# Performance work log

Hardware: AMD Instinct MI355X
Metric: run time of the kernel (lower is better)

Reference implementation:

```python
import jax, jax.numpy as jnp
import numpy as np

SEQ, D_IN, D_OUT = 8192, 768, 128


def setup_inputs() -> dict:
    key = jax.random.key(0)
    k1, k2, k3, k4 = jax.random.split(key, 4)
    x = jax.random.normal(k1, (SEQ, D_IN), dtype=jnp.float32)
    # torch nn.Linear weights are stored as [d_out, d_in]
    scale = 1.0 / np.sqrt(D_IN)
    w_query = jax.random.normal(k2, (D_OUT, D_IN), dtype=jnp.float32) * scale
    w_key = jax.random.normal(k3, (D_OUT, D_IN), dtype=jnp.float32) * scale
    w_value = jax.random.normal(k4, (D_OUT, D_IN), dtype=jnp.float32) * scale
    return {"x": x, "w_query": w_query, "w_key": w_key, "w_value": w_value}


def reference(x, w_query, w_key, w_value):
    # Linear with bias=False: y = x @ W.T   (W is [d_out, d_in])
    q = x @ w_query.T                      # [N, d_out]
    k = x @ w_key.T                        # [N, d_out]
    v = x @ w_value.T                      # [N, d_out]
    inv_sqrt_d = 1.0 / jnp.sqrt(jnp.float32(k.shape[-1]))
    scores = (q @ k.T) * inv_sqrt_d        # [N, N] -- fully materialized, as in source
    weights = jax.nn.softmax(scores, axis=-1)
    return weights @ v                     # [N, d_out]
```

## Files before the change

### kernel.cpp

```cpp
#include <hip/hip_runtime.h>
#include <stdint.h>

#define SEQ 8192
#define DIN 768
#define DOUT 128

typedef __attribute__((ext_vector_type(8))) short short8;
typedef __attribute__((ext_vector_type(8))) unsigned short ushort8v;
typedef __attribute__((ext_vector_type(4))) float f32x4;
typedef __attribute__((ext_vector_type(4))) unsigned int u32x4;

#define CEXPF (1.4426950408889634f * 0.08838834764831845f)

#if __has_builtin(__builtin_amdgcn_exp2f)
#define EXP2(x) __builtin_amdgcn_exp2f(x)
#else
#define EXP2(x) __builtin_exp2f(x)
#endif

__device__ __forceinline__ unsigned short f2bf(float f) {
  return (unsigned short)((__float_as_uint(f) + 0x8000u) >> 16);
}

__launch_bounds__(256, 2)
__global__ void qkv_kernel(const float* __restrict__ x,
                           const float* __restrict__ wq,
                           const float* __restrict__ wk,
                           const float* __restrict__ wvp,
                           unsigned short* __restrict__ Qb,
                           unsigned short* __restrict__ Kb,
                           unsigned short* __restrict__ Vtb) {
  __shared__ unsigned short smem[16640];
  unsigned short* xs  = smem;
  unsigned short* wsm = smem + 5120;

  const int t    = threadIdx.x;
  const int wid  = t >> 6;
  const int lane = t & 63;
  const int g    = lane >> 4;
  const int r    = lane & 15;
  const int z    = blockIdx.y;
  const int m0   = blockIdx.x * 128;
  const float* W = (z == 0) ? wq : (z == 1) ? wk : wvp;

  f32x4 acc[2][8];
#pragma unroll
  for (int i = 0; i < 2; i++)
#pragma unroll
    for (int j = 0; j < 8; j++) acc[i][j] = 0.f;

  const int srow = t >> 3;
  const int scol = (t & 7) * 4;

#pragma unroll 1
  for (int kb = 0; kb < DIN; kb += 32) {
    float4 xv[4], wv4[4];
#pragma unroll
    for (int u = 0; u < 4; u++) {
      int row = srow + u * 32;
      xv[u]  = *(const float4*)(x + (size_t)(m0 + row) * DIN + kb + scol);
      wv4[u] = *(const float4*)(W + (size_t)row * DIN + kb + scol);
    }
#pragma unroll
    for (int u = 0; u < 4; u++) {
      int row = srow + u * 32;
      ushort4 a, b;
      a.x = f2bf(xv[u].x);  a.y = f2bf(xv[u].y);
      a.z = f2bf(xv[u].z);  a.w = f2bf(xv[u].w);
      b.x = f2bf(wv4[u].x); b.y = f2bf(wv4[u].y);
      b.z = f2bf(wv4[u].z); b.w = f2bf(wv4[u].w);
      *(ushort4*)&xs[row * 40 + scol]  = a;
      *(ushort4*)&wsm[row * 40 + scol] = b;
    }
    __syncthreads();
    short8 af[2];
#pragma unroll
    for (int tm = 0; tm < 2; tm++)
      af[tm] = *(const short8*)&xs[(wid * 32 + tm * 16 + r) * 40 + g * 8];
#pragma unroll
    for (int tn = 0; tn < 8; tn++) {
      short8 bf = *(const short8*)&wsm[(tn * 16 + r) * 40 + g * 8];
      acc[0][tn] = __builtin_amdgcn_mfma_f32_16x16x32_bf16(af[0], bf, acc[0][tn], 0, 0, 0);
      acc[1][tn] = __builtin_amdgcn_mfma_f32_16x16x32_bf16(af[1], bf, acc[1][tn], 0, 0, 0);
    }
    __syncthreads();
  }

  if (z < 2) {
    unsigned short* out = (z == 0) ? Qb : Kb;
    const float sc = (z == 0) ? CEXPF : 1.0f;
#pragma unroll
    for (int tm = 0; tm < 2; tm++)
#pragma unroll
      for (int tn = 0; tn < 8; tn++)
#pragma unroll
        for (int rr = 0; rr < 4; rr++) {
          int row = m0 + wid * 32 + tm * 16 + g * 4 + rr;
          int col = tn * 16 + r;
          out[(size_t)row * DOUT + col] = f2bf(acc[tm][tn][rr] * sc);
        }
  } else {
    unsigned short* ct = smem;
#pragma unroll
    for (int tm = 0; tm < 2; tm++)
#pragma unroll
      for (int tn = 0; tn < 8; tn++)
#pragma unroll
        for (int rr = 0; rr < 4; rr++) {
          int m   = wid * 32 + tm * 16 + g * 4 + rr;
          int col = tn * 16 + r;
          ct[m * 130 + col] = f2bf(acc[tm][tn][rr]);
        }
    __syncthreads();
    int n  = t >> 1;
    int mh = (t & 1) * 64;
#pragma unroll
    for (int j = 0; j < 8; j++) {
      ushort8v vv;
#pragma unroll
      for (int i = 0; i < 8; i++) vv[i] = ct[(mh + j * 8 + i) * 130 + n];
      *(ushort8v*)(Vtb + (size_t)n * SEQ + m0 + mh + j * 8) = vv;
    }
  }
}

__launch_bounds__(256, 2)
__global__ void attn_kernel(const unsigned short* __restrict__ Qb,
                            const unsigned short* __restrict__ Kb,
                            const unsigned short* __restrict__ Vtb,
                            float* __restrict__ Opart,
                            float* __restrict__ lpart) {
  __shared__ unsigned char lds[51200];
  unsigned char* Kl = lds;
  unsigned char* Vl = lds + 16384;

  const int t    = threadIdx.x;
  const int wave = t >> 6;
  const int lane = t & 63;
  const int g    = lane >> 4;
  const int r    = lane & 15;
  unsigned short* Pl = (unsigned short*)(lds + 32768 + wave * 4608);

  const int qb = blockIdx.x;
  const int sp = blockIdx.y;
  const int q0 = qb * 128 + wave * 32;

  short8 qf[2][4];
#pragma unroll
  for (int s = 0; s < 2; s++)
#pragma unroll
    for (int c = 0; c < 4; c++)
      qf[s][c] = *(const short8*)(Qb + (size_t)(q0 + s * 16 + r) * DOUT + c * 32 + g * 8);

  short8 onesf;
#pragma unroll
  for (int j = 0; j < 8; j++) onesf[j] = (r == 0) ? (short)0x3F80 : (short)0;

  f32x4 oacc[2][8];
  f32x4 lacc[2];
#pragma unroll
  for (int s = 0; s < 2; s++) {
    lacc[s] = 0.f;
#pragma unroll
    for (int n = 0; n < 8; n++) oacc[s][n] = 0.f;
  }

#pragma unroll 1
  for (int it = 0; it < 16; it++) {
    const int kv0 = sp * 1024 + it * 64;
    {
      const u32x4* ksrc = (const u32x4*)(Kb + (size_t)kv0 * DOUT);
      u32x4 kv[4], vv[4];
#pragma unroll
      for (int j = 0; j < 4; j++) {
        int ci = t + 256 * j;
        kv[j] = ksrc[ci];
        int d = ci >> 3, cc = ci & 7;
        vv[j] = *(const u32x4*)(Vtb + (size_t)d * SEQ + kv0 + cc * 8);
      }
#pragma unroll
      for (int j = 0; j < 4; j++) {
        int ci = t + 256 * j;
        int row = ci >> 4, cc = ci & 15;
        *(u32x4*)(Kl + row * 256 + ((cc ^ (row & 15)) << 4)) = kv[j];
        int d = ci >> 3, c2 = ci & 7;
        *(u32x4*)(Vl + d * 128 + ((c2 ^ (d & 7)) << 4)) = vv[j];
      }
    }
    __syncthreads();

    f32x4 sf[2][4];
#pragma unroll
    for (int s = 0; s < 2; s++)
#pragma unroll
      for (int tt = 0; tt < 4; tt++) sf[s][tt] = 0.f;
#pragma unroll
    for (int tt = 0; tt < 4; tt++) {
      int row = tt * 16 + r;
#pragma unroll
      for (int c = 0; c < 4; c++) {
        int cc = c * 4 + g;
        short8 kf = *(const short8*)(Kl + row * 256 + ((cc ^ (row & 15)) << 4));
        sf[0][tt] = __builtin_amdgcn_mfma_f32_16x16x32_bf16(qf[0][c], kf, sf[0][tt], 0, 0, 0);
        sf[1][tt] = __builtin_amdgcn_mfma_f32_16x16x32_bf16(qf[1][c], kf, sf[1][tt], 0, 0, 0);
      }
    }

#pragma unroll
    for (int s = 0; s < 2; s++)
#pragma unroll
      for (int tt = 0; tt < 4; tt++)
#pragma unroll
        for (int rr = 0; rr < 4; rr++) {
          float p = EXP2(sf[s][tt][rr]);
          Pl[(s * 16 + g * 4 + rr) * 72 + tt * 16 + r] = f2bf(p);
        }
    short8 pf[2][2];
#pragma unroll
    for (int s = 0; s < 2; s++)
#pragma unroll
      for (int c2 = 0; c2 < 2; c2++)
        pf[s][c2] = *(const short8*)(Pl + (s * 16 + r) * 72 + c2 * 32 + g * 8);

#pragma unroll
    for (int nt = 0; nt < 8; nt++) {
      int d = nt * 16 + r;
#pragma unroll
      for (int c2 = 0; c2 < 2; c2++) {
        int cc = c2 * 4 + g;
        short8 vf = *(const short8*)(Vl + d * 128 + ((cc ^ (d & 7)) << 4));
        oacc[0][nt] = __builtin_amdgcn_mfma_f32_16x16x32_bf16(pf[0][c2], vf, oacc[0][nt], 0, 0, 0);
        oacc[1][nt] = __builtin_amdgcn_mfma_f32_16x16x32_bf16(pf[1][c2], vf, oacc[1][nt], 0, 0, 0);
      }
    }
#pragma unroll
    for (int s = 0; s < 2; s++) {
      lacc[s] = __builtin_amdgcn_mfma_f32_16x16x32_bf16(pf[s][0], onesf, lacc[s], 0, 0, 0);
      lacc[s] = __builtin_amdgcn_mfma_f32_16x16x32_bf16(pf[s][1], onesf, lacc[s], 0, 0, 0);
    }
    __syncthreads();
  }

  const size_t pbase = (size_t)sp * SEQ;
#pragma unroll
  for (int s = 0; s < 2; s++)
#pragma unroll
    for (int rr = 0; rr < 4; rr++) {
      int qrow = q0 + s * 16 + g * 4 + rr;
#pragma unroll
      for (int nt = 0; nt < 8; nt++)
        Opart[(pbase + qrow) * DOUT + nt * 16 + r] = oacc[s][nt][rr];
      if (r == 0) lpart[pbase + qrow] = lacc[s][rr];
    }
}

__global__ void combine_kernel(const float* __restrict__ Opart,
                               const float* __restrict__ lpart,
                               float* __restrict__ out) {
  int idx = blockIdx.x * 256 + threadIdx.x;
  int s   = idx >> 5;
  int d4  = (idx & 31) * 4;
  float L = 0.f;
  f32x4 acc = 0.f;
#pragma unroll
  for (int p = 0; p < 8; p++) {
    L += lpart[p * SEQ + s];
    acc += *(const f32x4*)(Opart + ((size_t)p * SEQ + s) * DOUT + d4);
  }
  f32x4 res = acc * (1.0f / L);
  *(f32x4*)(out + (size_t)s * DOUT + d4) = res;
}

extern "C" void kernel_launch(void* const* d_in, const int* in_sizes, int n_in,
                              void* d_out, int out_size, void* d_ws, size_t ws_size,
                              hipStream_t stream) {
  const float* x  = (const float*)d_in[0];
  const float* wq = (const float*)d_in[1];
  const float* wk = (const float*)d_in[2];
  const float* wv = (const float*)d_in[3];
  float* out = (float*)d_out;

  unsigned short* Qb  = (unsigned short*)d_ws;
  unsigned short* Kb  = Qb + (size_t)SEQ * DOUT;
  unsigned short* Vtb = Kb + (size_t)SEQ * DOUT;
  float* Opart = (float*)(Vtb + (size_t)SEQ * DOUT);
  float* lpart = Opart + (size_t)8 * SEQ * DOUT;
  if (ws_size < (size_t)(6291456 + 33554432 + 262144)) return;

  qkv_kernel<<<dim3(64, 3), 256, 0, stream>>>(x, wq, wk, wv, Qb, Kb, Vtb);
  attn_kernel<<<dim3(64, 8), 256, 0, stream>>>(Qb, Kb, Vtb, Opart, lpart);
  combine_kernel<<<dim3(1024), 256, 0, stream>>>(Opart, lpart, out);
}
```

Before: 149.0 us.

## Preconvert weights to bf16, retile QKV projection, use direct global-to-LDS loads in attention

Adds a small kernel that converts the three weight matrices to bf16 once per call, folding the softmax scale into Wq, and stores them in the Opart workspace before that buffer is reused. The QKV projection switches to 32-row tiles with a 256x3 grid and computes the transposed product, reading weight fragments straight from global memory. The attention kernel stages K and V with global_load_lds, swizzling on the global-address side, and swaps the QK^T operand order so P is written with vectorized stores. The intent is more parallelism in the projection, less fp32 weight traffic and conversion work, and fewer register round trips when loading K and V, at the cost of an extra kernel launch and repeated global reads of the weights.

Measured after the change: 136.4 us. 8.4% less time.

```diff
diff --git a/kernel.cpp b/kernel.cpp
--- a/kernel.cpp
+++ b/kernel.cpp
@@ -8,7 +8,6 @@
 typedef __attribute__((ext_vector_type(8))) short short8;
 typedef __attribute__((ext_vector_type(8))) unsigned short ushort8v;
 typedef __attribute__((ext_vector_type(4))) float f32x4;
-typedef __attribute__((ext_vector_type(4))) unsigned int u32x4;
 
 #define CEXPF (1.4426950408889634f * 0.08838834764831845f)
 
@@ -22,104 +21,109 @@
   return (unsigned short)((__float_as_uint(f) + 0x8000u) >> 16);
 }
 
-__launch_bounds__(256, 2)
+__device__ __forceinline__ void gload_lds16(const void* g, void* l) {
+  __builtin_amdgcn_global_load_lds(
+      (const __attribute__((address_space(1))) void*)g,
+      (__attribute__((address_space(3))) void*)l, 16, 0, 0);
+}
+
+__global__ void wconv_kernel(const float* __restrict__ wq,
+                             const float* __restrict__ wk,
+                             const float* __restrict__ wv,
+                             unsigned short* __restrict__ Wb) {
+  int idx4 = (blockIdx.x * 256 + threadIdx.x) * 4;
+  int z = idx4 / (DOUT * DIN);
+  int rem = idx4 - z * (DOUT * DIN);
+  const float* src = (z == 0) ? wq : (z == 1) ? wk : wv;
+  float4 v = *(const float4*)(src + rem);
+  float sc = (z == 0) ? CEXPF : 1.0f;
+  ushort4 o;
+  o.x = f2bf(v.x * sc); o.y = f2bf(v.y * sc);
+  o.z = f2bf(v.z * sc); o.w = f2bf(v.w * sc);
+  *(ushort4*)(Wb + idx4) = o;
+}
+
+__launch_bounds__(256, 3)
 __global__ void qkv_kernel(const float* __restrict__ x,
-                           const float* __restrict__ wq,
-                           const float* __restrict__ wk,
-                           const float* __restrict__ wvp,
+                           const unsigned short* __restrict__ Wb,
                            unsigned short* __restrict__ Qb,
                            unsigned short* __restrict__ Kb,
                            unsigned short* __restrict__ Vtb) {
-  __shared__ unsigned short smem[16640];
-  unsigned short* xs  = smem;
-  unsigned short* wsm = smem + 5120;
+  __shared__ unsigned short smem[4352];
+  unsigned short* xs = smem;
 
   const int t    = threadIdx.x;
-  const int wid  = t >> 6;
+  const int w    = t >> 6;
   const int lane = t & 63;
   const int g    = lane >> 4;
   const int r    = lane & 15;
   const int z    = blockIdx.y;
-  const int m0   = blockIdx.x * 128;
-  const float* W = (z == 0) ? wq : (z == 1) ? wk : wvp;
-
-  f32x4 acc[2][8];
+  const int m0   = blockIdx.x * 32;
+  const unsigned short* Wz = Wb + (size_t)z * DOUT * DIN;
+
+  f32x4 acc[2][2];
 #pragma unroll
   for (int i = 0; i < 2; i++)
 #pragma unroll
-    for (int j = 0; j < 8; j++) acc[i][j] = 0.f;
+    for (int j = 0; j < 2; j++) acc[i][j] = 0.f;
 
   const int srow = t >> 3;
   const int scol = (t & 7) * 4;
 
 #pragma unroll 1
   for (int kb = 0; kb < DIN; kb += 32) {
-    float4 xv[4], wv4[4];
-#pragma unroll
-    for (int u = 0; u < 4; u++) {
-      int row = srow + u * 32;
-      xv[u]  = *(const float4*)(x + (size_t)(m0 + row) * DIN + kb + scol);
-      wv4[u] = *(const float4*)(W + (size_t)row * DIN + kb + scol);
-    }
-#pragma unroll
-    for (int u = 0; u < 4; u++) {
-      int row = srow + u * 32;
-      ushort4 a, b;
-      a.x = f2bf(xv[u].x);  a.y = f2bf(xv[u].y);
-      a.z = f2bf(xv[u].z);  a.w = f2bf(xv[u].w);
-      b.x = f2bf(wv4[u].x); b.y = f2bf(wv4[u].y);
-      b.z = f2bf(wv4[u].z); b.w = f2bf(wv4[u].w);
-      *(ushort4*)&xs[row * 40 + scol]  = a;
-      *(ushort4*)&wsm[row * 40 + scol] = b;
-    }
-    __syncthreads();
     short8 af[2];
 #pragma unroll
-    for (int tm = 0; tm < 2; tm++)
-      af[tm] = *(const short8*)&xs[(wid * 32 + tm * 16 + r) * 40 + g * 8];
-#pragma unroll
-    for (int tn = 0; tn < 8; tn++) {
-      short8 bf = *(const short8*)&wsm[(tn * 16 + r) * 40 + g * 8];
-      acc[0][tn] = __builtin_amdgcn_mfma_f32_16x16x32_bf16(af[0], bf, acc[0][tn], 0, 0, 0);
-      acc[1][tn] = __builtin_amdgcn_mfma_f32_16x16x32_bf16(af[1], bf, acc[1][tn], 0, 0, 0);
-    }
+    for (int mt = 0; mt < 2; mt++)
+      af[mt] = *(const short8*)(Wz + (size_t)(w * 32 + mt * 16 + r) * DIN + kb + g * 8);
+    float4 xv = *(const float4*)(x + (size_t)(m0 + srow) * DIN + kb + scol);
+    ushort4 xb;
+    xb.x = f2bf(xv.x); xb.y = f2bf(xv.y); xb.z = f2bf(xv.z); xb.w = f2bf(xv.w);
+    *(ushort4*)&xs[srow * 40 + scol] = xb;
+    __syncthreads();
+    short8 bf[2];
+#pragma unroll
+    for (int nt = 0; nt < 2; nt++)
+      bf[nt] = *(const short8*)&xs[(nt * 16 + r) * 40 + g * 8];
+#pragma unroll
+    for (int mt = 0; mt < 2; mt++)
+#pragma unroll
+      for (int nt = 0; nt < 2; nt++)
+        acc[mt][nt] = __builtin_amdgcn_mfma_f32_16x16x32_bf16(af[mt], bf[nt], acc[mt][nt], 0, 0, 0);
     __syncthreads();
   }
 
   if (z < 2) {
     unsigned short* out = (z == 0) ? Qb : Kb;
-    const float sc = (z == 0) ? CEXPF : 1.0f;
-#pragma unroll
-    for (int tm = 0; tm < 2; tm++)
-#pragma unroll
-      for (int tn = 0; tn < 8; tn++)
-#pragma unroll
-        for (int rr = 0; rr < 4; rr++) {
-          int row = m0 + wid * 32 + tm * 16 + g * 4 + rr;
-          int col = tn * 16 + r;
-          out[(size_t)row * DOUT + col] = f2bf(acc[tm][tn][rr] * sc);
-        }
+#pragma unroll
+    for (int mt = 0; mt < 2; mt++)
+#pragma unroll
+      for (int nt = 0; nt < 2; nt++) {
+        ushort4 o;
+        o.x = f2bf(acc[mt][nt][0]); o.y = f2bf(acc[mt][nt][1]);
+        o.z = f2bf(acc[mt][nt][2]); o.w = f2bf(acc[mt][nt][3]);
+        *(ushort4*)(out + (size_t)(m0 + nt * 16 + r) * DOUT + w * 32 + mt * 16 + g * 4) = o;
+      }
   } else {
     unsigned short* ct = smem;
 #pragma unroll
-    for (int tm = 0; tm < 2; tm++)
-#pragma unroll
-      for (int tn = 0; tn < 8; tn++)
-#pragma unroll
-        for (int rr = 0; rr < 4; rr++) {
-          int m   = wid * 32 + tm * 16 + g * 4 + rr;
-          int col = tn * 16 + r;
-          ct[m * 130 + col] = f2bf(acc[tm][tn][rr]);
-        }
-    __syncthreads();
-    int n  = t >> 1;
-    int mh = (t & 1) * 64;
-#pragma unroll
-    for (int j = 0; j < 8; j++) {
-      ushort8v vv;
-#pragma unroll
-      for (int i = 0; i < 8; i++) vv[i] = ct[(mh + j * 8 + i) * 130 + n];
-      *(ushort8v*)(Vtb + (size_t)n * SEQ + m0 + mh + j * 8) = vv;
+    for (int mt = 0; mt < 2; mt++)
+#pragma unroll
+      for (int nt = 0; nt < 2; nt++) {
+        ushort4 o;
+        o.x = f2bf(acc[mt][nt][0]); o.y = f2bf(acc[mt][nt][1]);
+        o.z = f2bf(acc[mt][nt][2]); o.w = f2bf(acc[mt][nt][3]);
+        *(ushort4*)&ct[(nt * 16 + r) * 136 + w * 32 + mt * 16 + g * 4] = o;
+      }
+    __syncthreads();
+    int col  = t >> 1;
+    int half = (t & 1) * 16;
+#pragma unroll
+    for (int h2 = 0; h2 < 2; h2++) {
+      ushort8v a;
+#pragma unroll
+      for (int i = 0; i < 8; i++) a[i] = ct[(half + h2 * 8 + i) * 136 + col];
+      *(ushort8v*)(Vtb + (size_t)col * SEQ + m0 + half + h2 * 8) = a;
     }
   }
 }
@@ -147,10 +151,10 @@
 
   short8 qf[2][4];
 #pragma unroll
-  for (int s = 0; s < 2; s++)
-#pragma unroll
-    for (int c = 0; c < 4; c++)
-      qf[s][c] = *(const short8*)(Qb + (size_t)(q0 + s * 16 + r) * DOUT + c * 32 + g * 8);
+  for (int nt = 0; nt < 2; nt++)
+#pragma unroll
+    for (int kc = 0; kc < 4; kc++)
+      qf[nt][kc] = *(const short8*)(Qb + (size_t)(q0 + nt * 16 + r) * DOUT + kc * 32 + g * 8);
 
   short8 onesf;
 #pragma unroll
@@ -159,98 +163,89 @@
   f32x4 oacc[2][8];
   f32x4 lacc[2];
 #pragma unroll
-  for (int s = 0; s < 2; s++) {
-    lacc[s] = 0.f;
-#pragma unroll
-    for (int n = 0; n < 8; n++) oacc[s][n] = 0.f;
+  for (int st = 0; st < 2; st++) {
+    lacc[st] = 0.f;
+#pragma unroll
+    for (int n = 0; n < 8; n++) oacc[st][n] = 0.f;
   }
 
 #pragma unroll 1
   for (int it = 0; it < 16; it++) {
     const int kv0 = sp * 1024 + it * 64;
-    {
-      const u32x4* ksrc = (const u32x4*)(Kb + (size_t)kv0 * DOUT);
-      u32x4 kv[4], vv[4];
-#pragma unroll
-      for (int j = 0; j < 4; j++) {
-        int ci = t + 256 * j;
-        kv[j] = ksrc[ci];
-        int d = ci >> 3, cc = ci & 7;
-        vv[j] = *(const u32x4*)(Vtb + (size_t)d * SEQ + kv0 + cc * 8);
-      }
-#pragma unroll
-      for (int j = 0; j < 4; j++) {
-        int ci = t + 256 * j;
-        int row = ci >> 4, cc = ci & 15;
-        *(u32x4*)(Kl + row * 256 + ((cc ^ (row & 15)) << 4)) = kv[j];
-        int d = ci >> 3, c2 = ci & 7;
-        *(u32x4*)(Vl + d * 128 + ((c2 ^ (d & 7)) << 4)) = vv[j];
-      }
-    }
-    __syncthreads();
-
-    f32x4 sf[2][4];
-#pragma unroll
-    for (int s = 0; s < 2; s++)
-#pragma unroll
-      for (int tt = 0; tt < 4; tt++) sf[s][tt] = 0.f;
-#pragma unroll
-    for (int tt = 0; tt < 4; tt++) {
-      int row = tt * 16 + r;
-#pragma unroll
-      for (int c = 0; c < 4; c++) {
-        int cc = c * 4 + g;
-        short8 kf = *(const short8*)(Kl + row * 256 + ((cc ^ (row & 15)) << 4));
-        sf[0][tt] = __builtin_amdgcn_mfma_f32_16x16x32_bf16(qf[0][c], kf, sf[0][tt], 0, 0, 0);
-        sf[1][tt] = __builtin_amdgcn_mfma_f32_16x16x32_bf16(qf[1][c], kf, sf[1][tt], 0, 0, 0);
-      }
-    }
-
-#pragma unroll
-    for (int s = 0; s < 2; s++)
-#pragma unroll
-      for (int tt = 0; tt < 4; tt++)
-#pragma unroll
-        for (int rr = 0; rr < 4; rr++) {
-          float p = EXP2(sf[s][tt][rr]);
-          Pl[(s * 16 + g * 4 + rr) * 72 + tt * 16 + r] = f2bf(p);
-        }
+#pragma unroll
+    for (int c = 0; c < 4; c++) {
+      int idx = (wave * 4 + c) * 64 + lane;
+      int krow = idx >> 4, kch = idx & 15;
+      gload_lds16(Kb + ((size_t)(kv0 + krow) << 7) + ((kch ^ (krow & 15)) << 3),
+                  Kl + ((wave * 4 + c) << 10) + (lane << 4));
+      int d = idx >> 3, c2 = idx & 7;
+      gload_lds16(Vtb + (size_t)d * SEQ + kv0 + ((c2 ^ (d & 7)) << 3),
+                  Vl + ((wave * 4 + c) << 10) + (lane << 4));
+    }
+    __syncthreads();
+
+    f32x4 sf[4][2];
+#pragma unroll
+    for (int mt = 0; mt < 4; mt++)
+#pragma unroll
+      for (int nt = 0; nt < 2; nt++) sf[mt][nt] = 0.f;
+#pragma unroll
+    for (int mt = 0; mt < 4; mt++) {
+      int row = mt * 16 + r;
+#pragma unroll
+      for (int kc = 0; kc < 4; kc++) {
+        short8 kf = *(const short8*)(Kl + row * 256 + (((kc * 4 + g) ^ (row & 15)) << 4));
+        sf[mt][0] = __builtin_amdgcn_mfma_f32_16x16x32_bf16(kf, qf[0][kc], sf[mt][0], 0, 0, 0);
+        sf[mt][1] = __builtin_amdgcn_mfma_f32_16x16x32_bf16(kf, qf[1][kc], sf[mt][1], 0, 0, 0);
+      }
+    }
+
+#pragma unroll
+    for (int mt = 0; mt < 4; mt++)
+#pragma unroll
+      for (int nt = 0; nt < 2; nt++) {
+        ushort4 p;
+        p.x = f2bf(EXP2(sf[mt][nt][0]));
+        p.y = f2bf(EXP2(sf[mt][nt][1]));
+        p.z = f2bf(EXP2(sf[mt][nt][2]));
+        p.w = f2bf(EXP2(sf[mt][nt][3]));
+        *(ushort4*)(Pl + (nt * 16 + r) * 72 + mt * 16 + g * 4) = p;
+      }
     short8 pf[2][2];
 #pragma unroll
-    for (int s = 0; s < 2; s++)
+    for (int st = 0; st < 2; st++)
 #pragma unroll
       for (int c2 = 0; c2 < 2; c2++)
-        pf[s][c2] = *(const short8*)(Pl + (s * 16 + r) * 72 + c2 * 32 + g * 8);
+        pf[st][c2] = *(const short8*)(Pl + (st * 16 + r) * 72 + c2 * 32 + g * 8);
 
 #pragma unroll
     for (int nt = 0; nt < 8; nt++) {
       int d = nt * 16 + r;
 #pragma unroll
       for (int c2 = 0; c2 < 2; c2++) {
-        int cc = c2 * 4 + g;
-        short8 vf = *(const short8*)(Vl + d * 128 + ((cc ^ (d & 7)) << 4));
+        short8 vf = *(const short8*)(Vl + d * 128 + (((c2 * 4 + g) ^ (d & 7)) << 4));
         oacc[0][nt] = __builtin_amdgcn_mfma_f32_16x16x32_bf16(pf[0][c2], vf, oacc[0][nt], 0, 0, 0);
         oacc[1][nt] = __builtin_amdgcn_mfma_f32_16x16x32_bf16(pf[1][c2], vf, oacc[1][nt], 0, 0, 0);
       }
     }
 #pragma unroll
-    for (int s = 0; s < 2; s++) {
-      lacc[s] = __builtin_amdgcn_mfma_f32_16x16x32_bf16(pf[s][0], onesf, lacc[s], 0, 0, 0);
-      lacc[s] = __builtin_amdgcn_mfma_f32_16x16x32_bf16(pf[s][1], onesf, lacc[s], 0, 0, 0);
+    for (int st = 0; st < 2; st++) {
+      lacc[st] = __builtin_amdgcn_mfma_f32_16x16x32_bf16(pf[st][0], onesf, lacc[st], 0, 0, 0);
+      lacc[st] = __builtin_amdgcn_mfma_f32_16x16x32_bf16(pf[st][1], onesf, lacc[st], 0, 0, 0);
     }
     __syncthreads();
   }
 
   const size_t pbase = (size_t)sp * SEQ;
 #pragma unroll
-  for (int s = 0; s < 2; s++)
+  for (int st = 0; st < 2; st++)
 #pragma unroll
     for (int rr = 0; rr < 4; rr++) {
-      int qrow = q0 + s * 16 + g * 4 + rr;
+      int qrow = q0 + st * 16 + g * 4 + rr;
 #pragma unroll
       for (int nt = 0; nt < 8; nt++)
-        Opart[(pbase + qrow) * DOUT + nt * 16 + r] = oacc[s][nt][rr];
-      if (r == 0) lpart[pbase + qrow] = lacc[s][rr];
+        Opart[(pbase + qrow) * DOUT + nt * 16 + r] = oacc[st][nt][rr];
+      if (r == 0) lpart[pbase + qrow] = lacc[st][rr];
     }
 }
 
@@ -285,9 +280,11 @@
   unsigned short* Vtb = Kb + (size_t)SEQ * DOUT;
   float* Opart = (float*)(Vtb + (size_t)SEQ * DOUT);
   float* lpart = Opart + (size_t)8 * SEQ * DOUT;
+  unsigned short* Wb  = (unsigned short*)Opart;
   if (ws_size < (size_t)(6291456 + 33554432 + 262144)) return;
 
-  qkv_kernel<<<dim3(64, 3), 256, 0, stream>>>(x, wq, wk, wv, Qb, Kb, Vtb);
+  wconv_kernel<<<dim3(288), 256, 0, stream>>>(wq, wk, wv, Wb);
+  qkv_kernel<<<dim3(256, 3), 256, 0, stream>>>(x, Wb, Qb, Kb, Vtb);
   attn_kernel<<<dim3(64, 8), 256, 0, stream>>>(Qb, Kb, Vtb, Opart, lpart);
   combine_kernel<<<dim3(1024), 256, 0, stream>>>(Opart, lpart, out);
 }
```
